# Kernel tuning notes

Measured on AMD Instinct MI355X. Metric: run time of the kernel, lower is better.

## Reference

```python
import jax, jax.numpy as jnp
import numpy as np

EPS = 1e-5
N, DEG, D, L = 50000, 16, 128, 2  # nodes, max_neighbor, embed_size, gnn_layer


def _log_map_zero(y):
    # Poincare ball log map at origin: atanh(||y||) * y / ||y||, with clamps
    n = jnp.linalg.norm(y, axis=-1, keepdims=True)
    nc = jnp.clip(n, EPS, 1.0 - EPS)
    return y * (jnp.arctanh(nc) / nc)


def _exp_map_zero(v):
    # Poincare ball exp map at origin: tanh(||v||) * v / ||v||
    n = jnp.linalg.norm(v, axis=-1, keepdims=True)
    nc = jnp.maximum(n, EPS)
    return v * (jnp.tanh(nc) / nc)


def setup_inputs() -> dict:
    key = jax.random.key(0)
    k1, k2, k3, k4, k5 = jax.random.split(key, 5)
    node_repr = jax.random.normal(k1, (N, D), jnp.float32) * 0.1
    adj = jax.random.randint(k2, (N, DEG), 0, N)
    weight = jax.random.normal(k3, (N, DEG), jnp.float32)
    mask = jnp.ones((N, 1), jnp.float32)
    # per-relation, per-layer message weights (2 relations: pos / neg edges)
    scale = 1.0 / np.sqrt(D)
    W_pos = jax.random.normal(k4, (L, D, D), jnp.float32) * scale
    W_neg = jax.random.normal(k5, (L, D, D), jnp.float32) * scale
    return {"node_repr": node_repr, "adj": adj, "weight": weight,
            "mask": mask, "W_pos": W_pos, "W_neg": W_neg}


def reference(node_repr, adj, weight, mask, W_pos, W_neg):
    # split_graph_by_negative_edge
    pos_m = (weight > 0).astype(weight.dtype)
    neg_m = (weight < 0).astype(weight.dtype)
    adjs = (adj * pos_m.astype(adj.dtype), adj * neg_m.astype(adj.dtype))
    ws = (weight * pos_m, (-weight) * neg_m)
    Ws = (W_pos, W_neg)

    x = node_repr
    for step in range(L):
        x = (_log_map_zero(x) if step > 0 else x) * mask
        combined = jnp.zeros_like(x)
        for a, w, W in zip(adjs, ws, Ws):
            msg = (x @ W[step]) * mask                    # [N, D]
            nb = msg[a.reshape(-1)].reshape(N, DEG, D)    # neighbor gather
            combined = combined + jnp.sum(w[..., None] * nb, axis=1)
        combined = combined * mask                        # dropout identity (eval)
        x = _exp_map_zero(combined) * mask
        x = jax.nn.relu(x) * mask                         # poincare activation
    return x
```

## Files before the change

kernel.cpp:

```cpp
#include <hip/hip_runtime.h>
#include <math.h>

#define DD 128
#define DEG 16
#define TM 16
#define LDST 136
#define EPSV 1e-5f

typedef _Float16 half4_t __attribute__((ext_vector_type(4)));
typedef _Float16 half8_t __attribute__((ext_vector_type(8)));
typedef float    f32x4   __attribute__((ext_vector_type(4)));

__device__ __forceinline__ float fast_tanh_over(float n) {
    float e  = __expf(2.f * n);
    float th = 1.f - __fdividef(2.f, e + 1.f);
    return __fdividef(th, n);
}
__device__ __forceinline__ float fast_atanh_over(float n) {
    float r = 0.5f * __logf(__fdividef(1.f + n, 1.f - n));
    return __fdividef(r, n);
}

__global__ void prep(const float* __restrict__ x, const float* __restrict__ mask,
                     _Float16* __restrict__ x16, int n4, int xb,
                     const float* __restrict__ Wp, const float* __restrict__ Wn,
                     _Float16* __restrict__ WT)
{
    if ((int)blockIdx.x < xb) {
        int i = blockIdx.x * blockDim.x + threadIdx.x;
        if (i >= n4) return;
        float m = mask[i >> 5];
        float m2 = m * m;
        float4 v = ((const float4*)x)[i];
        half4_t h;
        h[0] = (_Float16)(v.x * m2); h[1] = (_Float16)(v.y * m2);
        h[2] = (_Float16)(v.z * m2); h[3] = (_Float16)(v.w * m2);
        ((half4_t*)x16)[i] = h;
    } else {
        int bid   = blockIdx.x - xb;
        int mat   = bid >> 3;
        int chunk = bid & 7;
        int l = mat >> 1, rel = mat & 1;
        const float* __restrict__ src = (rel ? Wn : Wp) + (size_t)l * DD * DD;
        _Float16* __restrict__ dst = WT + (size_t)mat * DD * DD;
        for (int o = chunk * 2048 + threadIdx.x; o < chunk * 2048 + 2048; o += 256) {
            int nn = o >> 7, kk = o & 127;
            dst[o] = (_Float16)src[kk * DD + nn];
        }
    }
}

__global__ __launch_bounds__(256, 2) void fused_layer(
    const _Float16* __restrict__ src16,
    const int*   __restrict__ adj, const float* __restrict__ wgt,
    const float* __restrict__ mask,
    const _Float16* __restrict__ WTp, const _Float16* __restrict__ WTn,
    float* __restrict__ dst_f32, _Float16* __restrict__ dst_f16,
    int n, int apply_logmap)
{
    __shared__ __align__(16) _Float16 aggP[TM][LDST];
    __shared__ __align__(16) _Float16 aggN[TM][LDST];
    __shared__ float partA[4][TM];
    __shared__ float partB[4][TM];

    const int row0 = blockIdx.x * TM;
    const int tid  = threadIdx.x;
    const int qw   = tid >> 4;
    const int l16  = tid & 15;

    float aP[8] = {0.f,0.f,0.f,0.f,0.f,0.f,0.f,0.f};
    float aN[8] = {0.f,0.f,0.f,0.f,0.f,0.f,0.f,0.f};
    const int node = row0 + qw;
    if (node < n) {
        const int*   __restrict__ arow = adj + (size_t)node * DEG;
        const float* __restrict__ wrow = wgt + (size_t)node * DEG;
        int   idxs[16];
        float ws[16];
        #pragma unroll
        for (int b = 0; b < 4; ++b) {
            int4   ia = ((const int4*)arow)[b];
            float4 wa = ((const float4*)wrow)[b];
            idxs[b*4+0] = ia.x; idxs[b*4+1] = ia.y; idxs[b*4+2] = ia.z; idxs[b*4+3] = ia.w;
            ws[b*4+0] = wa.x; ws[b*4+1] = wa.y; ws[b*4+2] = wa.z; ws[b*4+3] = wa.w;
        }
        half8_t v[16];
        #pragma unroll
        for (int j = 0; j < 16; ++j)
            v[j] = *(const half8_t*)(src16 + (size_t)idxs[j] * DD + l16 * 8);
        #pragma unroll
        for (int j = 0; j < 16; ++j) {
            float wp = fmaxf(ws[j], 0.f);
            float wn = fmaxf(-ws[j], 0.f);
            #pragma unroll
            for (int c = 0; c < 8; ++c) {
                float f = (float)v[j][c];
                aP[c] += wp * f;
                aN[c] += wn * f;
            }
        }
    }
    half8_t hP, hN;
    #pragma unroll
    for (int c = 0; c < 8; ++c) { hP[c] = (_Float16)aP[c]; hN[c] = (_Float16)aN[c]; }
    *(half8_t*)&aggP[qw][l16 * 8] = hP;
    *(half8_t*)&aggN[qw][l16 * 8] = hN;
    __syncthreads();

    const int wv2  = tid >> 6;
    const int l64  = tid & 63;
    const int l15  = l64 & 15;
    const int quad = l64 >> 4;

    half8_t aPf[4], aNf[4];
    #pragma unroll
    for (int kb = 0; kb < 4; ++kb) {
        aPf[kb] = *(const half8_t*)&aggP[l15][kb * 32 + quad * 8];
        aNf[kb] = *(const half8_t*)&aggN[l15][kb * 32 + quad * 8];
    }

    f32x4 acc[2];
    acc[0] = (f32x4){0.f, 0.f, 0.f, 0.f};
    acc[1] = (f32x4){0.f, 0.f, 0.f, 0.f};
    #pragma unroll
    for (int t = 0; t < 2; ++t) {
        const int nb = wv2 * 2 + t;
        const _Float16* bp = WTp + (size_t)(nb * 16 + l15) * DD + quad * 8;
        const _Float16* bn = WTn + (size_t)(nb * 16 + l15) * DD + quad * 8;
        #pragma unroll
        for (int kb = 0; kb < 4; ++kb) {
            acc[t] = __builtin_amdgcn_mfma_f32_16x16x32_f16(
                aPf[kb], *(const half8_t*)(bp + kb * 32), acc[t], 0, 0, 0);
            acc[t] = __builtin_amdgcn_mfma_f32_16x16x32_f16(
                aNf[kb], *(const half8_t*)(bn + kb * 32), acc[t], 0, 0, 0);
        }
    }

    float cv0[4], cv1[4], mr[4];
    #pragma unroll
    for (int r = 0; r < 4; ++r) {
        const int rl  = quad * 4 + r;
        const int row = row0 + rl;
        float m = (row < n) ? mask[row] : 0.f;
        mr[r] = m;
        float c0 = acc[0][r] * m, c1 = acc[1][r] * m;
        cv0[r] = c0; cv1[r] = c1;
        float p = c0 * c0 + c1 * c1;
        p += __shfl_xor(p, 1); p += __shfl_xor(p, 2);
        p += __shfl_xor(p, 4); p += __shfl_xor(p, 8);
        if (l15 == 0) partA[wv2][rl] = p;
    }
    __syncthreads();

    float x0[4], x1[4];
    #pragma unroll
    for (int r = 0; r < 4; ++r) {
        const int rl = quad * 4 + r;
        float c2 = partA[0][rl] + partA[1][rl] + partA[2][rl] + partA[3][rl];
        float nc = fmaxf(sqrtf(c2), EPSV);
        float sc = fast_tanh_over(nc);
        float m  = mr[r];
        float t0 = fmaxf(cv0[r] * sc * m, 0.f) * m;
        float t1 = fmaxf(cv1[r] * sc * m, 0.f) * m;
        x0[r] = t0; x1[r] = t1;
        if (apply_logmap) {
            float p = t0 * t0 + t1 * t1;
            p += __shfl_xor(p, 1); p += __shfl_xor(p, 2);
            p += __shfl_xor(p, 4); p += __shfl_xor(p, 8);
            if (l15 == 0) partB[wv2][rl] = p;
        }
    }

    if (apply_logmap) {
        __syncthreads();
        #pragma unroll
        for (int r = 0; r < 4; ++r) {
            const int rl  = quad * 4 + r;
            const int row = row0 + rl;
            if (row >= n) continue;
            float s2  = partB[0][rl] + partB[1][rl] + partB[2][rl] + partB[3][rl];
            float nc2 = fminf(fmaxf(sqrtf(s2), EPSV), 1.f - EPSV);
            float f = fast_atanh_over(nc2) * mr[r] * mr[r];
            _Float16* drow = dst_f16 + (size_t)row * DD + wv2 * 32 + l15;
            drow[0]  = (_Float16)(x0[r] * f);
            drow[16] = (_Float16)(x1[r] * f);
        }
    } else {
        #pragma unroll
        for (int r = 0; r < 4; ++r) {
            const int rl  = quad * 4 + r;
            const int row = row0 + rl;
            if (row >= n) continue;
            float* drow = dst_f32 + (size_t)row * DD + wv2 * 32 + l15;
            drow[0]  = x0[r];
            drow[16] = x1[r];
        }
    }
}

extern "C" void kernel_launch(void* const* d_in, const int* in_sizes, int n_in,
                              void* d_out, int out_size, void* d_ws, size_t ws_size,
                              hipStream_t stream)
{
    const float* node_repr = (const float*)d_in[0];
    const int*   adj       = (const int*)  d_in[1];
    const float* weight    = (const float*)d_in[2];
    const float* mask      = (const float*)d_in[3];
    const float* W_pos     = (const float*)d_in[4];
    const float* W_neg     = (const float*)d_in[5];

    const int n = in_sizes[0] / DD;

    _Float16* x16 = (_Float16*)d_ws;
    _Float16* y16 = x16 + (size_t)n * DD;
    _Float16* WT  = y16 + (size_t)n * DD;

    const int n4 = n * DD / 4;
    const int xb = (n4 + 255) / 256;
    prep<<<xb + 32, 256, 0, stream>>>(node_repr, mask, x16, n4, xb,
                                      W_pos, W_neg, WT);

    dim3 grid((n + TM - 1) / TM);
    fused_layer<<<grid, 256, 0, stream>>>(x16, adj, weight, mask,
                                          WT + 0 * DD * DD, WT + 1 * DD * DD,
                                          nullptr, y16, n, 1);
    fused_layer<<<grid, 256, 0, stream>>>(y16, adj, weight, mask,
                                          WT + 2 * DD * DD, WT + 3 * DD * DD,
                                          (float*)d_out, nullptr, n, 0);
}
```

Measured before the change: 187.4 us.

## Quantize gathered node features to int8 with per-column scales

```diff
diff --git a/kernel.cpp b/kernel.cpp
--- a/kernel.cpp
+++ b/kernel.cpp
@@ -10,6 +10,7 @@
 typedef _Float16 half4_t __attribute__((ext_vector_type(4)));
 typedef _Float16 half8_t __attribute__((ext_vector_type(8)));
 typedef float    f32x4   __attribute__((ext_vector_type(4)));
+typedef signed char char8_t __attribute__((ext_vector_type(8)));
 
 __device__ __forceinline__ float fast_tanh_over(float n) {
     float e  = __expf(2.f * n);
@@ -50,8 +51,48 @@
     }
 }
 
+__global__ void colmax_k(const _Float16* __restrict__ src,
+                         unsigned* __restrict__ cmax, int n)
+{
+    __shared__ float red[256];
+    const int c  = threadIdx.x & 127;
+    const int r0 = threadIdx.x >> 7;
+    float m = 0.f;
+    for (int r = blockIdx.x * 2 + r0; r < n; r += gridDim.x * 2)
+        m = fmaxf(m, fabsf((float)src[(size_t)r * DD + c]));
+    red[threadIdx.x] = m;
+    __syncthreads();
+    if (threadIdx.x < 128) {
+        m = fmaxf(red[threadIdx.x], red[threadIdx.x + 128]);
+        atomicMax(&cmax[c], __float_as_uint(m));
+    }
+}
+
+__global__ void quant_k(const _Float16* __restrict__ src,
+                        const unsigned* __restrict__ cmaxu,
+                        uint2* __restrict__ dst8, int ngrp)
+{
+    int i = blockIdx.x * 256 + threadIdx.x;
+    if (i >= ngrp) return;
+    half8_t h = ((const half8_t*)src)[i];
+    const float4 c0 = ((const float4*)cmaxu)[(i & 15) * 2];
+    const float4 c1 = ((const float4*)cmaxu)[(i & 15) * 2 + 1];
+    float cm[8] = {c0.x, c0.y, c0.z, c0.w, c1.x, c1.y, c1.z, c1.w};
+    int q[8];
+    #pragma unroll
+    for (int c = 0; c < 8; ++c) {
+        float qs = __fdividef(127.f, fmaxf(cm[c], 1e-20f));
+        float f  = (float)h[c] * qs;
+        q[c] = __float2int_rn(fminf(fmaxf(f, -127.f), 127.f));
+    }
+    unsigned lo = (q[0] & 255) | ((q[1] & 255) << 8) | ((q[2] & 255) << 16) | ((unsigned)(q[3] & 255) << 24);
+    unsigned hi = (q[4] & 255) | ((q[5] & 255) << 8) | ((q[6] & 255) << 16) | ((unsigned)(q[7] & 255) << 24);
+    dst8[i] = make_uint2(lo, hi);
+}
+
 __global__ __launch_bounds__(256, 2) void fused_layer(
-    const _Float16* __restrict__ src16,
+    const signed char* __restrict__ src8,
+    const unsigned*    __restrict__ cmaxu,
     const int*   __restrict__ adj, const float* __restrict__ wgt,
     const float* __restrict__ mask,
     const _Float16* __restrict__ WTp, const _Float16* __restrict__ WTn,
@@ -67,6 +108,13 @@
     const int tid  = threadIdx.x;
     const int qw   = tid >> 4;
     const int l16  = tid & 15;
+
+    const float4 dc0 = ((const float4*)cmaxu)[l16 * 2];
+    const float4 dc1 = ((const float4*)cmaxu)[l16 * 2 + 1];
+    const float ds[8] = {dc0.x * (1.f/127.f), dc0.y * (1.f/127.f),
+                         dc0.z * (1.f/127.f), dc0.w * (1.f/127.f),
+                         dc1.x * (1.f/127.f), dc1.y * (1.f/127.f),
+                         dc1.z * (1.f/127.f), dc1.w * (1.f/127.f)};
 
     float aP[8] = {0.f,0.f,0.f,0.f,0.f,0.f,0.f,0.f};
     float aN[8] = {0.f,0.f,0.f,0.f,0.f,0.f,0.f,0.f};
@@ -83,10 +131,10 @@
             idxs[b*4+0] = ia.x; idxs[b*4+1] = ia.y; idxs[b*4+2] = ia.z; idxs[b*4+3] = ia.w;
             ws[b*4+0] = wa.x; ws[b*4+1] = wa.y; ws[b*4+2] = wa.z; ws[b*4+3] = wa.w;
         }
-        half8_t v[16];
+        char8_t v[16];
         #pragma unroll
         for (int j = 0; j < 16; ++j)
-            v[j] = *(const half8_t*)(src16 + (size_t)idxs[j] * DD + l16 * 8);
+            v[j] = *(const char8_t*)(src8 + (size_t)idxs[j] * DD + l16 * 8);
         #pragma unroll
         for (int j = 0; j < 16; ++j) {
             float wp = fmaxf(ws[j], 0.f);
@@ -101,7 +149,10 @@
     }
     half8_t hP, hN;
     #pragma unroll
-    for (int c = 0; c < 8; ++c) { hP[c] = (_Float16)aP[c]; hN[c] = (_Float16)aN[c]; }
+    for (int c = 0; c < 8; ++c) {
+        hP[c] = (_Float16)(aP[c] * ds[c]);
+        hN[c] = (_Float16)(aN[c] * ds[c]);
+    }
     *(half8_t*)&aggP[qw][l16 * 8] = hP;
     *(half8_t*)&aggN[qw][l16 * 8] = hN;
     __syncthreads();
@@ -210,20 +261,32 @@
 
     const int n = in_sizes[0] / DD;
 
-    _Float16* x16 = (_Float16*)d_ws;
-    _Float16* y16 = x16 + (size_t)n * DD;
-    _Float16* WT  = y16 + (size_t)n * DD;
+    unsigned char* ws = (unsigned char*)d_ws;
+    _Float16*    bufA  = (_Float16*)ws;
+    signed char* buf8  = (signed char*)(ws + (size_t)n * DD * 2);
+    _Float16*    WT    = (_Float16*)(ws + (size_t)n * DD * 3);
+    unsigned*    cmaxX = (unsigned*)(ws + (size_t)n * DD * 3 + (size_t)4 * DD * DD * 2);
+    unsigned*    cmaxY = cmaxX + DD;
+
+    hipMemsetAsync(cmaxX, 0, 2 * DD * sizeof(unsigned), stream);
 
     const int n4 = n * DD / 4;
     const int xb = (n4 + 255) / 256;
-    prep<<<xb + 32, 256, 0, stream>>>(node_repr, mask, x16, n4, xb,
+    prep<<<xb + 32, 256, 0, stream>>>(node_repr, mask, bufA, n4, xb,
                                       W_pos, W_neg, WT);
 
+    const int ngrp = n * DD / 8;
+    const int qb   = (ngrp + 255) / 256;
     dim3 grid((n + TM - 1) / TM);
-    fused_layer<<<grid, 256, 0, stream>>>(x16, adj, weight, mask,
+
+    colmax_k<<<256, 256, 0, stream>>>(bufA, cmaxX, n);
+    quant_k<<<qb, 256, 0, stream>>>(bufA, cmaxX, (uint2*)buf8, ngrp);
+    fused_layer<<<grid, 256, 0, stream>>>(buf8, cmaxX, adj, weight, mask,
                                           WT + 0 * DD * DD, WT + 1 * DD * DD,
-                                          nullptr, y16, n, 1);
-    fused_layer<<<grid, 256, 0, stream>>>(y16, adj, weight, mask,
+                                          nullptr, bufA, n, 1);
+    colmax_k<<<256, 256, 0, stream>>>(bufA, cmaxY, n);
+    quant_k<<<qb, 256, 0, stream>>>(bufA, cmaxY, (uint2*)buf8, ngrp);
+    fused_layer<<<grid, 256, 0, stream>>>(buf8, cmaxY, adj, weight, mask,
                                           WT + 2 * DD * DD, WT + 3 * DD * DD,
                                           (float*)d_out, nullptr, n, 0);
 }
```

New measurement: 248.3 us. 1.33x slower.

## Quantize node features to int8 with per-row scales for neighbor gather

Applied to the files above, without the earlier changes.

```diff
diff --git a/kernel.cpp b/kernel.cpp
--- a/kernel.cpp
+++ b/kernel.cpp
@@ -7,9 +7,9 @@
 #define LDST 136
 #define EPSV 1e-5f
 
-typedef _Float16 half4_t __attribute__((ext_vector_type(4)));
 typedef _Float16 half8_t __attribute__((ext_vector_type(8)));
 typedef float    f32x4   __attribute__((ext_vector_type(4)));
+typedef signed char c16v __attribute__((ext_vector_type(16)));
 
 __device__ __forceinline__ float fast_tanh_over(float n) {
     float e  = __expf(2.f * n);
@@ -22,22 +22,35 @@
 }
 
 __global__ void prep(const float* __restrict__ x, const float* __restrict__ mask,
-                     _Float16* __restrict__ x16, int n4, int xb,
+                     signed char* __restrict__ x8, float* __restrict__ xsc, int nA,
                      const float* __restrict__ Wp, const float* __restrict__ Wn,
                      _Float16* __restrict__ WT)
 {
-    if ((int)blockIdx.x < xb) {
-        int i = blockIdx.x * blockDim.x + threadIdx.x;
-        if (i >= n4) return;
-        float m = mask[i >> 5];
+    if ((int)blockIdx.x < nA) {
+        const int r   = blockIdx.x * 16 + (threadIdx.x >> 4);
+        const int c16 = threadIdx.x & 15;
+        float m  = mask[r];
         float m2 = m * m;
-        float4 v = ((const float4*)x)[i];
-        half4_t h;
-        h[0] = (_Float16)(v.x * m2); h[1] = (_Float16)(v.y * m2);
-        h[2] = (_Float16)(v.z * m2); h[3] = (_Float16)(v.w * m2);
-        ((half4_t*)x16)[i] = h;
+        const float4* xp = (const float4*)(x + (size_t)r * DD + c16 * 8);
+        float4 a = xp[0], b = xp[1];
+        float v[8] = {a.x*m2, a.y*m2, a.z*m2, a.w*m2, b.x*m2, b.y*m2, b.z*m2, b.w*m2};
+        float mx = 0.f;
+        #pragma unroll
+        for (int c = 0; c < 8; ++c) mx = fmaxf(mx, fabsf(v[c]));
+        mx = fmaxf(mx, __shfl_xor(mx, 1));
+        mx = fmaxf(mx, __shfl_xor(mx, 2));
+        mx = fmaxf(mx, __shfl_xor(mx, 4));
+        mx = fmaxf(mx, __shfl_xor(mx, 8));
+        float qs = __fdividef(127.f, fmaxf(mx, 1e-20f));
+        int q[8];
+        #pragma unroll
+        for (int c = 0; c < 8; ++c) q[c] = __float2int_rn(v[c] * qs);
+        unsigned lo = (q[0]&255) | ((q[1]&255)<<8) | ((q[2]&255)<<16) | ((unsigned)(q[3]&255)<<24);
+        unsigned hi = (q[4]&255) | ((q[5]&255)<<8) | ((q[6]&255)<<16) | ((unsigned)(q[7]&255)<<24);
+        *(uint2*)(x8 + (size_t)r * DD + c16 * 8) = make_uint2(lo, hi);
+        if (c16 == 0) xsc[r] = mx * (1.f / 127.f);
     } else {
-        int bid   = blockIdx.x - xb;
+        int bid   = blockIdx.x - nA;
         int mat   = bid >> 3;
         int chunk = bid & 7;
         int l = mat >> 1, rel = mat & 1;
@@ -51,63 +64,84 @@
 }
 
 __global__ __launch_bounds__(256, 2) void fused_layer(
-    const _Float16* __restrict__ src16,
+    const signed char* __restrict__ src8,
+    const float* __restrict__ sscale,
     const int*   __restrict__ adj, const float* __restrict__ wgt,
     const float* __restrict__ mask,
     const _Float16* __restrict__ WTp, const _Float16* __restrict__ WTn,
-    float* __restrict__ dst_f32, _Float16* __restrict__ dst_f16,
+    float* __restrict__ dst_f32,
+    signed char* __restrict__ dst8, float* __restrict__ dst_scale,
     int n, int apply_logmap)
 {
     __shared__ __align__(16) _Float16 aggP[TM][LDST];
     __shared__ __align__(16) _Float16 aggN[TM][LDST];
+    __shared__ int   eidxS[TM][DEG];
+    __shared__ float ewgtS[TM][DEG];
+    __shared__ float msh[TM];
     __shared__ float partA[4][TM];
     __shared__ float partB[4][TM];
+    __shared__ float partC[4][TM];
 
     const int row0 = blockIdx.x * TM;
     const int tid  = threadIdx.x;
-    const int qw   = tid >> 4;
-    const int l16  = tid & 15;
-
-    float aP[8] = {0.f,0.f,0.f,0.f,0.f,0.f,0.f,0.f};
-    float aN[8] = {0.f,0.f,0.f,0.f,0.f,0.f,0.f,0.f};
-    const int node = row0 + qw;
-    if (node < n) {
-        const int*   __restrict__ arow = adj + (size_t)node * DEG;
-        const float* __restrict__ wrow = wgt + (size_t)node * DEG;
-        int   idxs[16];
-        float ws[16];
-        #pragma unroll
-        for (int b = 0; b < 4; ++b) {
-            int4   ia = ((const int4*)arow)[b];
-            float4 wa = ((const float4*)wrow)[b];
-            idxs[b*4+0] = ia.x; idxs[b*4+1] = ia.y; idxs[b*4+2] = ia.z; idxs[b*4+3] = ia.w;
-            ws[b*4+0] = wa.x; ws[b*4+1] = wa.y; ws[b*4+2] = wa.z; ws[b*4+3] = wa.w;
-        }
-        half8_t v[16];
-        #pragma unroll
-        for (int j = 0; j < 16; ++j)
-            v[j] = *(const half8_t*)(src16 + (size_t)idxs[j] * DD + l16 * 8);
-        #pragma unroll
-        for (int j = 0; j < 16; ++j) {
-            float wp = fmaxf(ws[j], 0.f);
-            float wn = fmaxf(-ws[j], 0.f);
-            #pragma unroll
-            for (int c = 0; c < 8; ++c) {
-                float f = (float)v[j][c];
-                aP[c] += wp * f;
-                aN[c] += wn * f;
-            }
-        }
-    }
-    half8_t hP, hN;
-    #pragma unroll
-    for (int c = 0; c < 8; ++c) { hP[c] = (_Float16)aP[c]; hN[c] = (_Float16)aN[c]; }
-    *(half8_t*)&aggP[qw][l16 * 8] = hP;
-    *(half8_t*)&aggN[qw][l16 * 8] = hN;
+
+    {
+        const int nd = tid >> 4, eg = tid & 15;
+        int   av = adj[(size_t)(row0 + nd) * DEG + eg];
+        float wv = wgt[(size_t)(row0 + nd) * DEG + eg];
+        float sv = sscale[av];
+        eidxS[nd][eg] = av;
+        ewgtS[nd][eg] = wv * sv;
+        if (tid < TM) msh[tid] = mask[row0 + tid];
+    }
     __syncthreads();
 
+    const int l64  = tid & 63;
+    const int node = (tid >> 6) * 4 + (l64 >> 4);
+    const int e    = (l64 >> 3) & 1;
+    const int g    = l64 & 7;
+
+    int   idxl[8];
+    float wl[8];
+    #pragma unroll
+    for (int j = 0; j < 8; ++j) {
+        idxl[j] = eidxS[node][2 * j + e];
+        wl[j]   = ewgtS[node][2 * j + e];
+    }
+
+    float aP[16], aN[16];
+    #pragma unroll
+    for (int c = 0; c < 16; ++c) { aP[c] = 0.f; aN[c] = 0.f; }
+    const signed char* __restrict__ srcg = src8 + g * 16;
+    #pragma unroll
+    for (int j = 0; j < 8; ++j) {
+        c16v v = *(const c16v*)(srcg + ((size_t)idxl[j] << 7));
+        float wp = fmaxf(wl[j], 0.f);
+        float wn = fmaxf(-wl[j], 0.f);
+        #pragma unroll
+        for (int c = 0; c < 16; ++c) {
+            float f = (float)v[c];
+            aP[c] += wp * f;
+            aN[c] += wn * f;
+        }
+    }
+    {
+        half8_t hP, hN;
+        #pragma unroll
+        for (int c = 0; c < 8; ++c) {
+            float ownP  = e ? aP[8 + c] : aP[c];
+            float sendP = e ? aP[c]     : aP[8 + c];
+            float ownN  = e ? aN[8 + c] : aN[c];
+            float sendN = e ? aN[c]     : aN[8 + c];
+            hP[c] = (_Float16)(ownP + __shfl_xor(sendP, 8));
+            hN[c] = (_Float16)(ownN + __shfl_xor(sendN, 8));
+        }
+        *(half8_t*)&aggP[node][g * 16 + e * 8] = hP;
+        *(half8_t*)&aggN[node][g * 16 + e * 8] = hN;
+    }
+    __syncthreads();
+
     const int wv2  = tid >> 6;
-    const int l64  = tid & 63;
     const int l15  = l64 & 15;
     const int quad = l64 >> 4;
 
@@ -140,7 +174,7 @@
     for (int r = 0; r < 4; ++r) {
         const int rl  = quad * 4 + r;
         const int row = row0 + rl;
-        float m = (row < n) ? mask[row] : 0.f;
+        float m = (row < n) ? msh[rl] : 0.f;
         mr[r] = m;
         float c0 = acc[0][r] * m, c1 = acc[1][r] * m;
         cv0[r] = c0; cv1[r] = c1;
@@ -172,17 +206,37 @@
 
     if (apply_logmap) {
         __syncthreads();
+        float y0r[4], y1r[4];
+        #pragma unroll
+        for (int r = 0; r < 4; ++r) {
+            const int rl = quad * 4 + r;
+            float s2  = partB[0][rl] + partB[1][rl] + partB[2][rl] + partB[3][rl];
+            float nc2 = fminf(fmaxf(sqrtf(s2), EPSV), 1.f - EPSV);
+            float f = fast_atanh_over(nc2) * mr[r] * mr[r];
+            float y0 = x0[r] * f, y1 = x1[r] * f;
+            y0r[r] = y0; y1r[r] = y1;
+            float mm = fmaxf(fabsf(y0), fabsf(y1));
+            mm = fmaxf(mm, __shfl_xor(mm, 1));
+            mm = fmaxf(mm, __shfl_xor(mm, 2));
+            mm = fmaxf(mm, __shfl_xor(mm, 4));
+            mm = fmaxf(mm, __shfl_xor(mm, 8));
+            if (l15 == 0) partC[wv2][rl] = mm;
+        }
+        __syncthreads();
         #pragma unroll
         for (int r = 0; r < 4; ++r) {
             const int rl  = quad * 4 + r;
             const int row = row0 + rl;
             if (row >= n) continue;
-            float s2  = partB[0][rl] + partB[1][rl] + partB[2][rl] + partB[3][rl];
-            float nc2 = fminf(fmaxf(sqrtf(s2), EPSV), 1.f - EPSV);
-            float f = fast_atanh_over(nc2) * mr[r] * mr[r];
-            _Float16* drow = dst_f16 + (size_t)row * DD + wv2 * 32 + l15;
-            drow[0]  = (_Float16)(x0[r] * f);
-            drow[16] = (_Float16)(x1[r] * f);
+            float rmax = fmaxf(fmaxf(partC[0][rl], partC[1][rl]),
+                               fmaxf(partC[2][rl], partC[3][rl]));
+            float qs = __fdividef(127.f, fmaxf(rmax, 1e-20f));
+            int q0 = __float2int_rn(y0r[r] * qs);
+            int q1 = __float2int_rn(y1r[r] * qs);
+            signed char* drow = dst8 + (size_t)row * DD + wv2 * 32 + l15;
+            drow[0]  = (signed char)q0;
+            drow[16] = (signed char)q1;
+            if (wv2 == 0 && l15 == 0) dst_scale[row] = rmax * (1.f / 127.f);
         }
     } else {
         #pragma unroll
@@ -210,20 +264,21 @@
 
     const int n = in_sizes[0] / DD;
 
-    _Float16* x16 = (_Float16*)d_ws;
-    _Float16* y16 = x16 + (size_t)n * DD;
-    _Float16* WT  = y16 + (size_t)n * DD;
-
-    const int n4 = n * DD / 4;
-    const int xb = (n4 + 255) / 256;
-    prep<<<xb + 32, 256, 0, stream>>>(node_repr, mask, x16, n4, xb,
+    signed char* x8  = (signed char*)d_ws;
+    signed char* y8  = x8 + (size_t)n * DD;
+    float*       xsc = (float*)(y8 + (size_t)n * DD);
+    float*       ysc = xsc + n;
+    _Float16*    WT  = (_Float16*)(ysc + n);
+
+    const int nA = n / 16;
+    prep<<<nA + 32, 256, 0, stream>>>(node_repr, mask, x8, xsc, nA,
                                       W_pos, W_neg, WT);
 
     dim3 grid((n + TM - 1) / TM);
-    fused_layer<<<grid, 256, 0, stream>>>(x16, adj, weight, mask,
+    fused_layer<<<grid, 256, 0, stream>>>(x8, xsc, adj, weight, mask,
                                           WT + 0 * DD * DD, WT + 1 * DD * DD,
-                                          nullptr, y16, n, 1);
-    fused_layer<<<grid, 256, 0, stream>>>(y16, adj, weight, mask,
+                                          nullptr, y8, ysc, n, 1);
+    fused_layer<<<grid, 256, 0, stream>>>(y8, ysc, adj, weight, mask,
                                           WT + 2 * DD * DD, WT + 3 * DD * DD,
-                                          (float*)d_out, nullptr, n, 0);
-}
+                                          (float*)d_out, nullptr, nullptr, n, 0);
+}
```

Result: faster. 180.0 us (-3.9%).
